# Kernel optimization log

Measured on AMD Instinct MI355X. Metric: run time of the kernel, lower is better.

Reference implementation:

```python
import jax, jax.numpy as jnp
import numpy as np

D_MODEL = 1024
N_HEADS = 16
D_HEAD = D_MODEL // N_HEADS
SCALE = 1.0 / float(np.sqrt(D_HEAD))


def setup_inputs() -> dict:
    key = jax.random.key(0)
    ks = jax.random.split(key, 6)
    B, T = 4, 2048
    x = jax.random.normal(ks[0], (B, T, D_MODEL), dtype=jnp.float32)
    # torch Linear weights are [out, in]; y = x @ W.T
    s = 1.0 / np.sqrt(D_MODEL)
    Wq = jax.random.uniform(ks[1], (D_MODEL, D_MODEL), jnp.float32, -s, s)
    Wk = jax.random.uniform(ks[2], (D_MODEL, D_MODEL), jnp.float32, -s, s)
    Wv = jax.random.uniform(ks[3], (D_MODEL, D_MODEL), jnp.float32, -s, s)
    Wo = jax.random.uniform(ks[4], (D_MODEL, D_MODEL), jnp.float32, -s, s)
    bo = jax.random.uniform(ks[5], (D_MODEL,), jnp.float32, -s, s)
    return {"x": x, "Wq": Wq, "Wk": Wk, "Wv": Wv, "Wo": Wo, "bo": bo}


def reference(x, Wq, Wk, Wv, Wo, bo):
    B, T, D = x.shape
    # QKV projections (torch Linear: x @ W.T), split into heads -> [B, H, T, d]
    def heads(y):
        return y.reshape(B, T, N_HEADS, D_HEAD).transpose(0, 2, 1, 3)
    q = heads(x @ Wq.T)
    k = heads(x @ Wk.T)
    v = heads(x @ Wv.T)
    scores = jnp.einsum("bhqd,bhkd->bhqk", q, k) * SCALE  # [B,H,T,T]
    probs = jax.nn.softmax(scores, axis=-1)
    # dropout is identity in eval/inference mode
    out = jnp.einsum("bhqk,bhkd->bhqd", probs, v)  # [B,H,T,d]
    out = out.transpose(0, 2, 1, 3).reshape(B, T, D)
    return out @ Wo.T + bo
```

## Files before the change

kernel.cpp:

```cpp
#include <hip/hip_runtime.h>
#include <stdint.h>

#define D_MODEL 1024
#define NH 16
#define DH 64
#define TSEQ 2048
#define BATCH 4
#define MTOT (BATCH*TSEQ)
#define NQ (MTOT*D_MODEL)
#define WSZ (D_MODEL*D_MODEL)
#define QSCALE 0.18033688f

typedef __attribute__((ext_vector_type(8))) short bf16x8;
typedef __attribute__((ext_vector_type(8))) unsigned short u16x8;
typedef __attribute__((ext_vector_type(4))) float f32x4;
typedef __attribute__((ext_vector_type(2))) float f32x2;
typedef unsigned short u16;
typedef unsigned int u32;

__device__ __forceinline__ void gl_lds16(const void* g, void* l) {
  __builtin_amdgcn_global_load_lds(
      (__attribute__((address_space(1))) void*)g,
      (__attribute__((address_space(3))) void*)l, 16, 0, 0);
}
__device__ __forceinline__ u16 f2bf(float f) {
  u32 u = __builtin_bit_cast(u32, f);
  u = u + 0x7fffu + ((u >> 16) & 1u);
  return (u16)(u >> 16);
}
__device__ __forceinline__ float bf2f(u16 b) {
  u32 u = ((u32)b) << 16;
  return __builtin_bit_cast(float, u);
}

__device__ __forceinline__ void exp2pk4(const f32x4 s, float& e0, float& e1,
                                        float& e2, float& e3, u32& pk01,
                                        u32& pk23) {
  asm("v_exp_f32 %0, %6\n\t"
      "v_exp_f32 %1, %7\n\t"
      "v_exp_f32 %2, %8\n\t"
      "v_exp_f32 %3, %9\n\t"
      "s_nop 1\n\t"
      "v_cvt_pk_bf16_f32 %4, %0, %1\n\t"
      "v_cvt_pk_bf16_f32 %5, %2, %3"
      : "=&v"(e0), "=&v"(e1), "=&v"(e2), "=&v"(e3), "=&v"(pk01), "=&v"(pk23)
      : "v"(s[0]), "v"(s[1]), "v"(s[2]), "v"(s[3]));
}

__global__ __launch_bounds__(256) void detect_dtype(
    const u32* __restrict__ wq_raw, int* __restrict__ flag)
{
  __shared__ int cnt;
  if (threadIdx.x == 0) cnt = 0;
  __syncthreads();
  int c = 0;
  for (int i = threadIdx.x; i < 2048; i += 256) {
    const u32 e = (wq_raw[i] >> 7) & 0xFFu;
    if (e >= 90u && e <= 126u) ++c;
  }
  atomicAdd(&cnt, c);
  __syncthreads();
  if (threadIdx.x == 0) *flag = (cnt > 1024) ? 1 : 0;
}

__global__ __launch_bounds__(256) void convert_inputs(
    const void* __restrict__ x, const void* __restrict__ wq,
    const void* __restrict__ wk, const void* __restrict__ wv,
    const void* __restrict__ wo,
    u16* __restrict__ xb, u16* __restrict__ wqb, u16* __restrict__ wkb,
    u16* __restrict__ wvb, u16* __restrict__ wob,
    const int* __restrict__ flag_p)
{
  if (*flag_p) return;
  const int seg = blockIdx.y;
  const void* src; u16* dst; int n;
  switch (seg) {
    case 0:  src = x;  dst = xb;  n = NQ;  break;
    case 1:  src = wq; dst = wqb; n = WSZ; break;
    case 2:  src = wk; dst = wkb; n = WSZ; break;
    case 3:  src = wv; dst = wvb; n = WSZ; break;
    default: src = wo; dst = wob; n = WSZ; break;
  }
  const int idx = (blockIdx.x * 256 + threadIdx.x) * 8;
  if (idx >= n) return;
  const float4 f0 = *(const float4*)((const float*)src + idx);
  const float4 f1 = *(const float4*)((const float*)src + idx + 4);
  union { u16 s[8]; u16x8 v; } u;
  u.s[0] = f2bf(f0.x); u.s[1] = f2bf(f0.y); u.s[2] = f2bf(f0.z); u.s[3] = f2bf(f0.w);
  u.s[4] = f2bf(f1.x); u.s[5] = f2bf(f1.y); u.s[6] = f2bf(f1.z); u.s[7] = f2bf(f1.w);
  *(u16x8*)(dst + idx) = u.v;
}

__global__ __launch_bounds__(256, 2) void qkv_gemm(
    const int* __restrict__ flag_p, const u16* __restrict__ x_raw,
    u16* __restrict__ dout,
    const u16* __restrict__ Wq, const u16* __restrict__ Wk,
    const u16* __restrict__ Wv,
    const void* __restrict__ wq_r, const void* __restrict__ wk_r,
    const void* __restrict__ wv_r,
    u16* __restrict__ Ko, u16* __restrict__ VTo)
{
  __shared__ __align__(16) u16 As [2 * 128 * 32];
  __shared__ __align__(16) u16 Bqs[2 * 128 * 32];
  __shared__ __align__(16) u16 Bks[2 * 128 * 32];
  __shared__ __align__(16) u16 Bvs[2 * 128 * 32];
  const int flag = *flag_p;
  const u16* __restrict__ X  = flag ? x_raw : dout;
  u16* __restrict__ QTo = flag ? dout : dout + NQ;
  const u16* __restrict__ WQ = flag ? (const u16*)wq_r : Wq;
  const u16* __restrict__ WK = flag ? (const u16*)wk_r : Wk;
  const u16* __restrict__ WV = flag ? (const u16*)wv_r : Wv;
  const int t = threadIdx.x;
  const int m0 = blockIdx.x * 128;
  const int n0 = blockIdx.y * 128;
  const int wave = t >> 6, lane = t & 63;
  const int wm = (wave >> 1) * 64, wn = (wave & 1) * 64;
  const int lr = lane & 15, g = lane >> 4, kg = g * 8;

  const int srow0 = t >> 2, skc = (t & 3) * 8;
  const int srow1 = srow0 + 64;
  const u16* a0 = X  + (size_t)(m0 + srow0) * D_MODEL + skc;
  const u16* a1 = X  + (size_t)(m0 + srow1) * D_MODEL + skc;
  const u16* q0p = WQ + (size_t)(n0 + srow0) * D_MODEL + skc;
  const u16* q1p = WQ + (size_t)(n0 + srow1) * D_MODEL + skc;
  const u16* k0p = WK + (size_t)(n0 + srow0) * D_MODEL + skc;
  const u16* k1p = WK + (size_t)(n0 + srow1) * D_MODEL + skc;
  const u16* v0p = WV + (size_t)(n0 + srow0) * D_MODEL + skc;
  const u16* v1p = WV + (size_t)(n0 + srow1) * D_MODEL + skc;

  f32x4 accq[4][4] = {};
  f32x4 acck[4][4] = {};
  f32x4 accv[4][4] = {};

  for (int kt = 0; kt < D_MODEL / 64; ++kt) {
    gl_lds16(a0,       &As [t * 8]);
    gl_lds16(a1,       &As [(t + 256) * 8]);
    gl_lds16(a0 + 32,  &As [4096 + t * 8]);
    gl_lds16(a1 + 32,  &As [4096 + (t + 256) * 8]);
    gl_lds16(q0p,      &Bqs[t * 8]);
    gl_lds16(q1p,      &Bqs[(t + 256) * 8]);
    gl_lds16(q0p + 32, &Bqs[4096 + t * 8]);
    gl_lds16(q1p + 32, &Bqs[4096 + (t + 256) * 8]);
    gl_lds16(k0p,      &Bks[t * 8]);
    gl_lds16(k1p,      &Bks[(t + 256) * 8]);
    gl_lds16(k0p + 32, &Bks[4096 + t * 8]);
    gl_lds16(k1p + 32, &Bks[4096 + (t + 256) * 8]);
    gl_lds16(v0p,      &Bvs[t * 8]);
    gl_lds16(v1p,      &Bvs[(t + 256) * 8]);
    gl_lds16(v0p + 32, &Bvs[4096 + t * 8]);
    gl_lds16(v1p + 32, &Bvs[4096 + (t + 256) * 8]);
    a0 += 64; a1 += 64; q0p += 64; q1p += 64;
    k0p += 64; k1p += 64; v0p += 64; v1p += 64;
    __syncthreads();
#pragma unroll
    for (int h = 0; h < 2; ++h) {
      bf16x8 af[4], bfr[4];
#pragma unroll
      for (int i = 0; i < 4; ++i)
        af[i] = *(const bf16x8*)&As[h * 4096 + (wm + i * 16 + lr) * 32 + kg];
#pragma unroll
      for (int j = 0; j < 4; ++j)
        bfr[j] = *(const bf16x8*)&Bqs[h * 4096 + (wn + j * 16 + lr) * 32 + kg];
#pragma unroll
      for (int i = 0; i < 4; ++i)
#pragma unroll
        for (int j = 0; j < 4; ++j)
          accq[i][j] = __builtin_amdgcn_mfma_f32_16x16x32_bf16(af[i], bfr[j], accq[i][j], 0, 0, 0);
#pragma unroll
      for (int j = 0; j < 4; ++j)
        bfr[j] = *(const bf16x8*)&Bks[h * 4096 + (wn + j * 16 + lr) * 32 + kg];
#pragma unroll
      for (int j = 0; j < 4; ++j)
#pragma unroll
        for (int i = 0; i < 4; ++i)
          acck[j][i] = __builtin_amdgcn_mfma_f32_16x16x32_bf16(bfr[j], af[i], acck[j][i], 0, 0, 0);
#pragma unroll
      for (int j = 0; j < 4; ++j)
        bfr[j] = *(const bf16x8*)&Bvs[h * 4096 + (wn + j * 16 + lr) * 32 + kg];
#pragma unroll
      for (int i = 0; i < 4; ++i)
#pragma unroll
        for (int j = 0; j < 4; ++j)
          accv[i][j] = __builtin_amdgcn_mfma_f32_16x16x32_bf16(af[i], bfr[j], accv[i][j], 0, 0, 0);
    }
    __syncthreads();
  }

  const int bidx = m0 >> 11;
#pragma unroll
  for (int zz = 0; zz < 2; ++zz) {
    u16* O = zz ? VTo : QTo;
    const float sc = zz ? 1.0f : QSCALE;
#pragma unroll
    for (int i = 0; i < 4; ++i) {
      const int rowg = m0 + wm + i * 16 + (g << 2);
      const int tq = rowg & (TSEQ - 1);
#pragma unroll
      for (int j = 0; j < 4; ++j) {
        const int colg = n0 + wn + j * 16 + lr;
        const int h = colg >> 6, d = colg & 63;
        const f32x4 a = zz ? accv[i][j] : accq[i][j];
        union { u16 s[4]; uint2 v; } u;
#pragma unroll
        for (int r = 0; r < 4; ++r) u.s[r] = f2bf(a[r] * sc);
        *(uint2*)&O[((size_t)(bidx * NH + h) * DH + d) * TSEQ + tq] = u.v;
      }
    }
  }
#pragma unroll
  for (int j = 0; j < 4; ++j) {
    const int dg = n0 + wn + j * 16 + (g << 2);
    const int hh = dg >> 6, d0 = dg & 63;
#pragma unroll
    for (int i = 0; i < 4; ++i) {
      const int tg = m0 + wm + i * 16 + lr;
      const int tq = tg & (TSEQ - 1);
      union { u16 s[4]; uint2 v; } u;
#pragma unroll
      for (int r = 0; r < 4; ++r) u.s[r] = f2bf(acck[j][i][r]);
      *(uint2*)&Ko[((size_t)(bidx * NH + hh) * TSEQ + tq) * DH + d0] = u.v;
    }
  }
}

__global__ __launch_bounds__(256) void flash_attn(
    const int* __restrict__ flag_p, const u16* __restrict__ dout,
    const u16* __restrict__ K, const u16* __restrict__ VT,
    u16* __restrict__ AO)
{
  __shared__ __align__(16) u16 Ks[2][2 * 64 * 32];
  __shared__ __align__(16) u16 Vs[2][2 * 64 * 32];
  __shared__ __align__(16) u16 Ps[4 * 64 * 72];
  __shared__ float Ls[4 * 64];
  const int flag = *flag_p;
  const u16* __restrict__ QT = flag ? dout : dout + NQ;
  const int t = threadIdx.x;
  const int wave = t >> 6, lane = t & 63;
  const int lr = lane & 15, g = lane >> 4, kg = g * 8;
  const int bh = blockIdx.x;
  const int q0 = blockIdx.y * 256;
  const u16* __restrict__ QTh = QT + (size_t)bh * DH * TSEQ;
  const u16* __restrict__ Kh = K + (size_t)bh * TSEQ * DH;
  const u16* __restrict__ Vh = VT + (size_t)bh * DH * TSEQ;

  const int qi = q0 + wave * 64 + lr;
  bf16x8 qf[8];
#pragma unroll
  for (int s = 0; s < 4; ++s) {
    union { u16 v[8]; bf16x8 b; } u0, u1;
#pragma unroll
    for (int j = 0; j < 8; ++j) {
      u0.v[j] = QTh[(size_t)(kg + j) * TSEQ + qi + s * 16];
      u1.v[j] = QTh[(size_t)(32 + kg + j) * TSEQ + qi + s * 16];
    }
    qf[s * 2] = u0.b; qf[s * 2 + 1] = u1.b;
  }

  f32x4 acc[4][4] = {};
  f32x2 ls0[4] = {}, ls1[4] = {};

  const int srow = t >> 2, skc = (t & 3) * 8;
  const u16* kb = Kh + (size_t)srow * DH + skc;
  const u16* vb = Vh + (size_t)srow * TSEQ + skc;
  u16* const pw = &Ps[wave * 64 * 72];

  gl_lds16(kb,      &Ks[0][t * 8]);
  gl_lds16(kb + 32, &Ks[0][(t + 256) * 8]);
  gl_lds16(vb,      &Vs[0][t * 8]);
  gl_lds16(vb + 32, &Vs[0][(t + 256) * 8]);
  kb += 64 * DH; vb += 64;

  int cur = 0;
  for (int j0 = 0; j0 < TSEQ; j0 += 64) {
    __syncthreads();
    if (j0 + 64 < TSEQ) {
      gl_lds16(kb,      &Ks[cur ^ 1][t * 8]);
      gl_lds16(kb + 32, &Ks[cur ^ 1][(t + 256) * 8]);
      gl_lds16(vb,      &Vs[cur ^ 1][t * 8]);
      gl_lds16(vb + 32, &Vs[cur ^ 1][(t + 256) * 8]);
      kb += 64 * DH; vb += 64;
    }
    const u16* __restrict__ Kc = Ks[cur];
    const u16* __restrict__ Vc = Vs[cur];

#pragma unroll
    for (int jn = 0; jn < 2; ++jn) {
      const bf16x8 kf0 = *(const bf16x8*)&Kc[(jn * 16 + lr) * 32 + kg];
      const bf16x8 kf1 = *(const bf16x8*)&Kc[2048 + (jn * 16 + lr) * 32 + kg];
#pragma unroll
      for (int s = 0; s < 4; ++s) {
        f32x4 sS = {};
        sS = __builtin_amdgcn_mfma_f32_16x16x32_bf16(kf0, qf[s * 2],     sS, 0, 0, 0);
        sS = __builtin_amdgcn_mfma_f32_16x16x32_bf16(kf1, qf[s * 2 + 1], sS, 0, 0, 0);
        float e0, e1, e2, e3;
        uint2 w;
        exp2pk4(sS, e0, e1, e2, e3, w.x, w.y);
        ls0[s] += (f32x2){e0, e1};
        ls1[s] += (f32x2){e2, e3};
        *(uint2*)&pw[s * 16 * 72 + lr * 72 + jn * 16 + g * 4] = w;
      }
    }

    bf16x8 pf0[4];
#pragma unroll
    for (int s = 0; s < 4; ++s)
      pf0[s] = *(const bf16x8*)&pw[s * 16 * 72 + lr * 72 + kg];

#pragma unroll
    for (int jn = 2; jn < 4; ++jn) {
      const bf16x8 kf0 = *(const bf16x8*)&Kc[(jn * 16 + lr) * 32 + kg];
      const bf16x8 kf1 = *(const bf16x8*)&Kc[2048 + (jn * 16 + lr) * 32 + kg];
#pragma unroll
      for (int s = 0; s < 4; ++s) {
        f32x4 sS = {};
        sS = __builtin_amdgcn_mfma_f32_16x16x32_bf16(kf0, qf[s * 2],     sS, 0, 0, 0);
        sS = __builtin_amdgcn_mfma_f32_16x16x32_bf16(kf1, qf[s * 2 + 1], sS, 0, 0, 0);
        float e0, e1, e2, e3;
        uint2 w;
        exp2pk4(sS, e0, e1, e2, e3, w.x, w.y);
        ls0[s] += (f32x2){e0, e1};
        ls1[s] += (f32x2){e2, e3};
        *(uint2*)&pw[s * 16 * 72 + lr * 72 + jn * 16 + g * 4] = w;
      }
    }

#pragma unroll
    for (int dn = 0; dn < 4; ++dn) {
      const bf16x8 vf0 = *(const bf16x8*)&Vc[(dn * 16 + lr) * 32 + kg];
#pragma unroll
      for (int s = 0; s < 4; ++s)
        acc[s][dn] = __builtin_amdgcn_mfma_f32_16x16x32_bf16(pf0[s], vf0, acc[s][dn], 0, 0, 0);
    }

    bf16x8 pf1[4];
#pragma unroll
    for (int s = 0; s < 4; ++s)
      pf1[s] = *(const bf16x8*)&pw[s * 16 * 72 + lr * 72 + 32 + kg];
#pragma unroll
    for (int dn = 0; dn < 4; ++dn) {
      const bf16x8 vf1 = *(const bf16x8*)&Vc[2048 + (dn * 16 + lr) * 32 + kg];
#pragma unroll
      for (int s = 0; s < 4; ++s)
        acc[s][dn] = __builtin_amdgcn_mfma_f32_16x16x32_bf16(pf1[s], vf1, acc[s][dn], 0, 0, 0);
    }
    cur ^= 1;
  }

#pragma unroll
  for (int s = 0; s < 4; ++s) {
    float l = (ls0[s][0] + ls0[s][1]) + (ls1[s][0] + ls1[s][1]);
    l += __shfl_xor(l, 16, 64);
    l += __shfl_xor(l, 32, 64);
    Ls[wave * 64 + s * 16 + lr] = l;
  }
  __syncthreads();

  const int bb = bh >> 4, hh = bh & 15;
#pragma unroll
  for (int s = 0; s < 4; ++s) {
#pragma unroll
    for (int r = 0; r < 4; ++r) {
      const int qq = g * 4 + r;
      const float inv = 1.f / fmaxf(Ls[wave * 64 + s * 16 + qq], 1e-30f);
      const int ti = q0 + wave * 64 + s * 16 + qq;
      u16* dst = AO + (((size_t)bb * TSEQ + ti) * NH + hh) * DH + lr;
#pragma unroll
      for (int dn = 0; dn < 4; ++dn)
        dst[dn * 16] = f2bf(acc[s][dn][r] * inv);
    }
  }
}

__global__ __launch_bounds__(256) void out_gemm(
    const int* __restrict__ flag_p,
    const u16* __restrict__ A, const u16* __restrict__ W,
    const void* __restrict__ wo_r,
    const void* __restrict__ bias_raw, void* __restrict__ outp)
{
  __shared__ __align__(16) u16 As[2 * 128 * 32];
  __shared__ __align__(16) u16 Bs[2 * 128 * 32];
  const int flag = *flag_p;
  const u16* __restrict__ Wm = flag ? (const u16*)wo_r : W;
  const int t = threadIdx.x;
  const int m0 = blockIdx.x * 128;
  const int n0 = blockIdx.y * 128;
  const int wave = t >> 6, lane = t & 63;
  const int wm = (wave >> 1) * 64, wn = (wave & 1) * 64;
  const int lr = lane & 15, kg = (lane >> 4) * 8;

  const int srow0 = t >> 2, skc = (t & 3) * 8;
  const int srow1 = srow0 + 64;
  const u16* a0 = A + (size_t)(m0 + srow0) * D_MODEL + skc;
  const u16* a1 = A + (size_t)(m0 + srow1) * D_MODEL + skc;
  const u16* b0 = Wm + (size_t)(n0 + srow0) * D_MODEL + skc;
  const u16* b1 = Wm + (size_t)(n0 + srow1) * D_MODEL + skc;

  f32x4 acc[4][4] = {};

  for (int kt = 0; kt < D_MODEL / 64; ++kt) {
    gl_lds16(a0,      &As[t * 8]);
    gl_lds16(a1,      &As[(t + 256) * 8]);
    gl_lds16(a0 + 32, &As[4096 + t * 8]);
    gl_lds16(a1 + 32, &As[4096 + (t + 256) * 8]);
    gl_lds16(b0,      &Bs[t * 8]);
    gl_lds16(b1,      &Bs[(t + 256) * 8]);
    gl_lds16(b0 + 32, &Bs[4096 + t * 8]);
    gl_lds16(b1 + 32, &Bs[4096 + (t + 256) * 8]);
    a0 += 64; a1 += 64; b0 += 64; b1 += 64;
    __syncthreads();
#pragma unroll
    for (int h = 0; h < 2; ++h) {
      bf16x8 af[4], bfr[4];
#pragma unroll
      for (int i = 0; i < 4; ++i)
        af[i] = *(const bf16x8*)&As[h * 4096 + (wm + i * 16 + lr) * 32 + kg];
#pragma unroll
      for (int j = 0; j < 4; ++j)
        bfr[j] = *(const bf16x8*)&Bs[h * 4096 + (wn + j * 16 + lr) * 32 + kg];
#pragma unroll
      for (int i = 0; i < 4; ++i)
#pragma unroll
        for (int j = 0; j < 4; ++j)
          acc[i][j] = __builtin_amdgcn_mfma_f32_16x16x32_bf16(af[i], bfr[j], acc[i][j], 0, 0, 0);
    }
    __syncthreads();
  }

#pragma unroll
  for (int j = 0; j < 4; ++j) {
    const int colg = n0 + wn + j * 16 + lr;
    const float bv = flag ? bf2f(((const u16*)bias_raw)[colg])
                          : ((const float*)bias_raw)[colg];
#pragma unroll
    for (int i = 0; i < 4; ++i) {
      const int rowg = m0 + wm + i * 16 + ((lane >> 4) << 2);
      if (flag) {
        u16* dst = (u16*)outp + (size_t)rowg * D_MODEL + colg;
#pragma unroll
        for (int r = 0; r < 4; ++r)
          dst[(size_t)r * D_MODEL] = f2bf(acc[i][j][r] + bv);
      } else {
        float* dst = (float*)outp + (size_t)rowg * D_MODEL + colg;
#pragma unroll
        for (int r = 0; r < 4; ++r)
          dst[(size_t)r * D_MODEL] = acc[i][j][r] + bv;
      }
    }
  }
}

extern "C" void kernel_launch(void* const* d_in, const int* in_sizes, int n_in,
                              void* d_out, int out_size, void* d_ws, size_t ws_size,
                              hipStream_t stream) {
  const void* x  = d_in[0];
  const void* wq = d_in[1];
  const void* wk = d_in[2];
  const void* wv = d_in[3];
  const void* wo = d_in[4];
  const void* bo = d_in[5];
  u16* dout = (u16*)d_out;

  int* flag = (int*)d_ws;
  u16* wqb = (u16*)d_ws + 8;
  u16* wkb = wqb + WSZ;
  u16* wvb = wkb + WSZ;
  u16* wob = wvb + WSZ;
  u16* kk  = wob + WSZ;
  u16* vt  = kk + NQ;
  u16* ao  = vt + NQ;

  detect_dtype<<<1, 256, 0, stream>>>((const u32*)wq, flag);

  dim3 gc(NQ / (256 * 8), 5);
  convert_inputs<<<gc, dim3(256), 0, stream>>>(
      x, wq, wk, wv, wo, dout, wqb, wkb, wvb, wob, flag);

  dim3 g1(MTOT / 128, D_MODEL / 128, 1);
  qkv_gemm<<<g1, dim3(256), 0, stream>>>(
      flag, (const u16*)x, dout, wqb, wkb, wvb, wq, wk, wv, kk, vt);

  dim3 g2(BATCH * NH, TSEQ / 256, 1);
  flash_attn<<<g2, dim3(256), 0, stream>>>(flag, dout, kk, vt, ao);

  dim3 g3(MTOT / 128, D_MODEL / 128, 1);
  out_gemm<<<g3, dim3(256), 0, stream>>>(flag, ao, wob, wo, bo, d_out);
}
```

Measured before the change: 268.3 us.

## Double-buffer QKV GEMM LDS tiles to overlap global loads with MFMA

The QKV projection loop previously loaded a 64-wide K slab into LDS, synced, computed, and synced again, leaving loads and compute serialized. It now uses two 32-wide LDS buffers: the next slab is prefetched into the alternate buffer while MFMAs consume the current one, with one barrier per iteration. This hides global-load latency, but doubles the iteration count and barriers per K element. Correctness relies on the single barrier at the top of each iteration, with global_load_lds completion assumed to be handled by the compiler's waitcnt before that barrier.

New measurement: 290.2 us. +8.2%, slower.

```diff
diff --git a/kernel.cpp b/kernel.cpp
--- a/kernel.cpp
+++ b/kernel.cpp
@@ -100,10 +100,10 @@
     const void* __restrict__ wv_r,
     u16* __restrict__ Ko, u16* __restrict__ VTo)
 {
-  __shared__ __align__(16) u16 As [2 * 128 * 32];
-  __shared__ __align__(16) u16 Bqs[2 * 128 * 32];
-  __shared__ __align__(16) u16 Bks[2 * 128 * 32];
-  __shared__ __align__(16) u16 Bvs[2 * 128 * 32];
+  __shared__ __align__(16) u16 As [2][128 * 32];
+  __shared__ __align__(16) u16 Bqs[2][128 * 32];
+  __shared__ __align__(16) u16 Bks[2][128 * 32];
+  __shared__ __align__(16) u16 Bvs[2][128 * 32];
   const int flag = *flag_p;
   const u16* __restrict__ X  = flag ? x_raw : dout;
   u16* __restrict__ QTo = flag ? dout : dout + NQ;
@@ -132,58 +132,61 @@
   f32x4 acck[4][4] = {};
   f32x4 accv[4][4] = {};
 
-  for (int kt = 0; kt < D_MODEL / 64; ++kt) {
-    gl_lds16(a0,       &As [t * 8]);
-    gl_lds16(a1,       &As [(t + 256) * 8]);
-    gl_lds16(a0 + 32,  &As [4096 + t * 8]);
-    gl_lds16(a1 + 32,  &As [4096 + (t + 256) * 8]);
-    gl_lds16(q0p,      &Bqs[t * 8]);
-    gl_lds16(q1p,      &Bqs[(t + 256) * 8]);
-    gl_lds16(q0p + 32, &Bqs[4096 + t * 8]);
-    gl_lds16(q1p + 32, &Bqs[4096 + (t + 256) * 8]);
-    gl_lds16(k0p,      &Bks[t * 8]);
-    gl_lds16(k1p,      &Bks[(t + 256) * 8]);
-    gl_lds16(k0p + 32, &Bks[4096 + t * 8]);
-    gl_lds16(k1p + 32, &Bks[4096 + (t + 256) * 8]);
-    gl_lds16(v0p,      &Bvs[t * 8]);
-    gl_lds16(v1p,      &Bvs[(t + 256) * 8]);
-    gl_lds16(v0p + 32, &Bvs[4096 + t * 8]);
-    gl_lds16(v1p + 32, &Bvs[4096 + (t + 256) * 8]);
-    a0 += 64; a1 += 64; q0p += 64; q1p += 64;
-    k0p += 64; k1p += 64; v0p += 64; v1p += 64;
+  gl_lds16(a0,  &As [0][t * 8]);
+  gl_lds16(a1,  &As [0][(t + 256) * 8]);
+  gl_lds16(q0p, &Bqs[0][t * 8]);
+  gl_lds16(q1p, &Bqs[0][(t + 256) * 8]);
+  gl_lds16(k0p, &Bks[0][t * 8]);
+  gl_lds16(k1p, &Bks[0][(t + 256) * 8]);
+  gl_lds16(v0p, &Bvs[0][t * 8]);
+  gl_lds16(v1p, &Bvs[0][(t + 256) * 8]);
+  a0 += 32; a1 += 32; q0p += 32; q1p += 32;
+  k0p += 32; k1p += 32; v0p += 32; v1p += 32;
+
+  int cur = 0;
+  for (int kt = 0; kt < D_MODEL / 32; ++kt) {
     __syncthreads();
-#pragma unroll
-    for (int h = 0; h < 2; ++h) {
-      bf16x8 af[4], bfr[4];
+    if (kt + 1 < D_MODEL / 32) {
+      gl_lds16(a0,  &As [cur ^ 1][t * 8]);
+      gl_lds16(a1,  &As [cur ^ 1][(t + 256) * 8]);
+      gl_lds16(q0p, &Bqs[cur ^ 1][t * 8]);
+      gl_lds16(q1p, &Bqs[cur ^ 1][(t + 256) * 8]);
+      gl_lds16(k0p, &Bks[cur ^ 1][t * 8]);
+      gl_lds16(k1p, &Bks[cur ^ 1][(t + 256) * 8]);
+      gl_lds16(v0p, &Bvs[cur ^ 1][t * 8]);
+      gl_lds16(v1p, &Bvs[cur ^ 1][(t + 256) * 8]);
+      a0 += 32; a1 += 32; q0p += 32; q1p += 32;
+      k0p += 32; k1p += 32; v0p += 32; v1p += 32;
+    }
+    bf16x8 af[4], bfr[4];
+#pragma unroll
+    for (int i = 0; i < 4; ++i)
+      af[i] = *(const bf16x8*)&As[cur][(wm + i * 16 + lr) * 32 + kg];
+#pragma unroll
+    for (int j = 0; j < 4; ++j)
+      bfr[j] = *(const bf16x8*)&Bqs[cur][(wn + j * 16 + lr) * 32 + kg];
+#pragma unroll
+    for (int i = 0; i < 4; ++i)
+#pragma unroll
+      for (int j = 0; j < 4; ++j)
+        accq[i][j] = __builtin_amdgcn_mfma_f32_16x16x32_bf16(af[i], bfr[j], accq[i][j], 0, 0, 0);
+#pragma unroll
+    for (int j = 0; j < 4; ++j)
+      bfr[j] = *(const bf16x8*)&Bks[cur][(wn + j * 16 + lr) * 32 + kg];
+#pragma unroll
+    for (int j = 0; j < 4; ++j)
 #pragma unroll
       for (int i = 0; i < 4; ++i)
-        af[i] = *(const bf16x8*)&As[h * 4096 + (wm + i * 16 + lr) * 32 + kg];
+        acck[j][i] = __builtin_amdgcn_mfma_f32_16x16x32_bf16(bfr[j], af[i], acck[j][i], 0, 0, 0);
+#pragma unroll
+    for (int j = 0; j < 4; ++j)
+      bfr[j] = *(const bf16x8*)&Bvs[cur][(wn + j * 16 + lr) * 32 + kg];
+#pragma unroll
+    for (int i = 0; i < 4; ++i)
 #pragma unroll
       for (int j = 0; j < 4; ++j)
-        bfr[j] = *(const bf16x8*)&Bqs[h * 4096 + (wn + j * 16 + lr) * 32 + kg];
-#pragma unroll
-      for (int i = 0; i < 4; ++i)
-#pragma unroll
-        for (int j = 0; j < 4; ++j)
-          accq[i][j] = __builtin_amdgcn_mfma_f32_16x16x32_bf16(af[i], bfr[j], accq[i][j], 0, 0, 0);
-#pragma unroll
-      for (int j = 0; j < 4; ++j)
-        bfr[j] = *(const bf16x8*)&Bks[h * 4096 + (wn + j * 16 + lr) * 32 + kg];
-#pragma unroll
-      for (int j = 0; j < 4; ++j)
-#pragma unroll
-        for (int i = 0; i < 4; ++i)
-          acck[j][i] = __builtin_amdgcn_mfma_f32_16x16x32_bf16(bfr[j], af[i], acck[j][i], 0, 0, 0);
-#pragma unroll
-      for (int j = 0; j < 4; ++j)
-        bfr[j] = *(const bf16x8*)&Bvs[h * 4096 + (wn + j * 16 + lr) * 32 + kg];
-#pragma unroll
-      for (int i = 0; i < 4; ++i)
-#pragma unroll
-        for (int j = 0; j < 4; ++j)
-          accv[i][j] = __builtin_amdgcn_mfma_f32_16x16x32_bf16(af[i], bfr[j], accv[i][j], 0, 0, 0);
-    }
-    __syncthreads();
+        accv[i][j] = __builtin_amdgcn_mfma_f32_16x16x32_bf16(af[i], bfr[j], accv[i][j], 0, 0, 0);
+    cur ^= 1;
   }
 
   const int bidx = m0 >> 11;
```
